# Optimization experiments

Hardware: AMD Instinct MI355X
Metric: run time of the kernel (lower is better)

The kernel has to match this reference:

```python
import math
import jax, jax.numpy as jnp
import numpy as np

H = 16  # head_count

def setup_inputs() -> dict:
    key = jax.random.key(0)
    ks = jax.random.split(key, 7)
    B, S, D = 2, 2048, 1024
    query = jax.random.normal(ks[0], (B, S, D), dtype=jnp.float32)
    # mask: True = masked position (matches masked_fill_ semantics)
    mask = jax.random.randint(ks[1], (B, S, S), 0, 2) > 0
    scale = 1.0 / math.sqrt(D)  # xavier-ish init scale
    Wq = jax.random.normal(ks[2], (D, D), dtype=jnp.float32) * scale
    Wk = jax.random.normal(ks[3], (D, D), dtype=jnp.float32) * scale
    Wv = jax.random.normal(ks[4], (D, D), dtype=jnp.float32) * scale
    Wo = jax.random.normal(ks[5], (D, D), dtype=jnp.float32) * scale
    bo = jnp.zeros((D,), dtype=jnp.float32)
    return {"query": query, "mask": mask, "Wq": Wq, "Wk": Wk, "Wv": Wv, "Wo": Wo, "bo": bo}


def reference(query, mask, Wq, Wk, Wv, Wo, bo):
    B, S, D = query.shape
    dh = D // H

    def split_heads(x):  # [B,S,D] -> [B,H,S,dh]
        return x.reshape(B, S, H, dh).transpose(0, 2, 1, 3)

    # torch nn.Linear computes x @ W.T (bias-free for q/k/v)
    q = split_heads(query @ Wq.T) * (1.0 / math.sqrt(dh))
    k = split_heads(query @ Wk.T)
    v = split_heads(query @ Wv.T)

    scores = jnp.einsum('bhqd,bhkd->bhqk', q, k)           # [B,H,S,S]
    scores = jnp.where(mask[:, None, :, :], jnp.float32(-1e18), scores)
    weights = jax.nn.softmax(scores, axis=-1)               # dropout=0 -> identity
    ctx = jnp.einsum('bhqk,bhkd->bhqd', weights, v)         # [B,H,S,dh]
    ctx = ctx.transpose(0, 2, 1, 3).reshape(B, S, D)        # combine heads
    return ctx @ Wo.T + bo
```

## Files before the change

### kernel.cpp

```cpp
#include <hip/hip_runtime.h>

#define S_LEN 2048
#define D_MODEL 1024
#define NH 16
#define DH 64

typedef __bf16 bf16x8 __attribute__((ext_vector_type(8)));
typedef __bf16 bf16x4 __attribute__((ext_vector_type(4)));
typedef float f32x4 __attribute__((ext_vector_type(4)));

__device__ __forceinline__ unsigned short f2bf(float f) {
  unsigned int x = __float_as_uint(f);
  x += 0x7fffu + ((x >> 16) & 1u);
  return (unsigned short)(x >> 16);
}

__device__ __forceinline__ bf16x4 cvt4(f32x4 v) {
  return __builtin_convertvector(v, bf16x4);
}

__device__ __forceinline__ float exp2raw(float x) {
#if __has_builtin(__builtin_amdgcn_exp2f)
  return __builtin_amdgcn_exp2f(x);
#else
  return exp2f(x);
#endif
}

__device__ __forceinline__ f32x4 mfma16(bf16x8 a, bf16x8 b, f32x4 c) {
  return __builtin_amdgcn_mfma_f32_16x16x32_bf16(a, b, c, 0, 0, 0);
}

__device__ __forceinline__ void gl2lds(const unsigned short* g, unsigned short* l) {
  __builtin_amdgcn_global_load_lds(
      (__attribute__((address_space(1))) void*)g,
      (__attribute__((address_space(3))) void*)l, 16, 0, 0);
}

__global__ __launch_bounds__(256) void prep_kernel(
    const float* __restrict__ q, const float* __restrict__ wq,
    const float* __restrict__ wk, const float* __restrict__ wv,
    const float* __restrict__ wo, const int* __restrict__ mask,
    unsigned short* __restrict__ qbf, unsigned short* __restrict__ wbf,
    unsigned long long* __restrict__ bits) {
  const int bx = blockIdx.x;
  if (bx < 32768) {
    int i = bx * 256 + threadIdx.x;
    unsigned long long bal = __ballot(mask[i] != 0);
    if ((threadIdx.x & 63) == 0) bits[i >> 6] = bal;
  } else {
    const long t = (long)(bx - 32768) * 256 + threadIdx.x;
    const float* src;
    unsigned short* dst;
    long e;
    if (t < 524288) { src = q; dst = qbf; e = t * 8; }
    else {
      long u = t - 524288;
      int wi = (int)(u >> 17);
      e = (u & 131071) * 8;
      src = wi == 0 ? wq : wi == 1 ? wk : wi == 2 ? wv : wo;
      dst = wbf + (long)wi * 1048576;
    }
    float4 a = *(const float4*)(src + e);
    float4 b = *(const float4*)(src + e + 4);
    ushort4 p0 = {f2bf(a.x), f2bf(a.y), f2bf(a.z), f2bf(a.w)};
    ushort4 p1 = {f2bf(b.x), f2bf(b.y), f2bf(b.z), f2bf(b.w)};
    *(ushort4*)(dst + e) = p0;
    *(ushort4*)(dst + e + 4) = p1;
  }
}

__global__ __launch_bounds__(256) void gemm_qkv(
    const unsigned short* __restrict__ A, const unsigned short* __restrict__ W3,
    unsigned short* __restrict__ qb, unsigned short* __restrict__ kb,
    unsigned short* __restrict__ vt, float qscale) {
  __shared__ unsigned short As[128 * 64];
  __shared__ unsigned short Bs[128 * 64];
  const int tid = threadIdx.x, lane = tid & 63, wid = tid >> 6;
  const int wm = wid >> 1, wn = wid & 1;
  const int quad = lane >> 4, c = lane & 15, cx = c & 7;
  const int nG = blockIdx.x * 128;
  const int wi = nG >> 10, nn0 = nG & 1023;
  const int m0 = blockIdx.y * 128;
  const unsigned short* Bsrc = W3 + (size_t)wi * 1048576;
  const int srow = lane >> 3;
  const int schk = ((lane & 7) ^ srow) * 8;
  const unsigned short* ag = A + (size_t)(m0 + wid * 32 + srow) * 1024 + schk;
  const unsigned short* bg = Bsrc + (size_t)(nn0 + wid * 32 + srow) * 1024 + schk;
  f32x4 acc[4][4] = {};
  for (int kk = 0; kk < 1024; kk += 64) {
#pragma unroll
    for (int i = 0; i < 4; ++i) {
      gl2lds(ag + (size_t)(i * 8) * 1024 + kk, &As[(wid * 32 + i * 8) * 64]);
      gl2lds(bg + (size_t)(i * 8) * 1024 + kk, &Bs[(wid * 32 + i * 8) * 64]);
    }
    __syncthreads();
#pragma unroll
    for (int kc = 0; kc < 2; ++kc) {
      bf16x8 a[4], b[4];
#pragma unroll
      for (int mt = 0; mt < 4; ++mt)
        a[mt] = *(const bf16x8*)(
            &As[(wm * 64 + mt * 16 + c) * 64 + ((kc * 4 + quad) ^ cx) * 8]);
#pragma unroll
      for (int nt = 0; nt < 4; ++nt)
        b[nt] = *(const bf16x8*)(
            &Bs[(wn * 64 + nt * 16 + c) * 64 + ((kc * 4 + quad) ^ cx) * 8]);
#pragma unroll
      for (int mt = 0; mt < 4; ++mt)
#pragma unroll
        for (int nt = 0; nt < 4; ++nt)
          acc[mt][nt] = mfma16(a[mt], b[nt], acc[mt][nt]);
    }
    __syncthreads();
  }
#pragma unroll
  for (int mt = 0; mt < 4; ++mt) {
#pragma unroll
    for (int nt = 0; nt < 4; ++nt) {
      const int mb = m0 + wm * 64 + mt * 16 + quad * 4;
      const int n = nn0 + wn * 64 + nt * 16 + c;
      const int hh = n >> 6, d = n & 63;
      const int bb = mb >> 11, ss = mb & 2047;
      if (wi == 0) {
#pragma unroll
        for (int r = 0; r < 4; ++r)
          qb[(size_t)((bb * NH + hh) * S_LEN + ss + r) * DH + d] =
              f2bf(acc[mt][nt][r] * qscale);
      } else if (wi == 1) {
#pragma unroll
        for (int r = 0; r < 4; ++r)
          kb[(size_t)((bb * NH + hh) * S_LEN + ss + r) * DH + d] =
              f2bf(acc[mt][nt][r]);
      } else {
        *(bf16x4*)(vt + (size_t)((bb * NH + hh) * DH + d) * S_LEN + ss) =
            cvt4(acc[mt][nt]);
      }
    }
  }
}

__global__ __launch_bounds__(256) void gemm_out(
    const unsigned short* __restrict__ A, const unsigned short* __restrict__ W,
    float* __restrict__ out, const float* __restrict__ bias) {
  __shared__ unsigned short As[128 * 64];
  __shared__ unsigned short Bs[64 * 64];
  const int tid = threadIdx.x, lane = tid & 63, wid = tid >> 6;
  const int wm = wid >> 1, wn = wid & 1;
  const int quad = lane >> 4, c = lane & 15, cx = c & 7;
  const int n0 = blockIdx.x * 64, m0 = blockIdx.y * 128;
  const int srow = lane >> 3;
  const int schk = ((lane & 7) ^ srow) * 8;
  const unsigned short* ag = A + (size_t)(m0 + wid * 32 + srow) * 1024 + schk;
  const unsigned short* bg = W + (size_t)(n0 + wid * 16 + srow) * 1024 + schk;
  f32x4 acc[4][2] = {};
  for (int kk = 0; kk < 1024; kk += 64) {
#pragma unroll
    for (int i = 0; i < 4; ++i)
      gl2lds(ag + (size_t)(i * 8) * 1024 + kk, &As[(wid * 32 + i * 8) * 64]);
#pragma unroll
    for (int i = 0; i < 2; ++i)
      gl2lds(bg + (size_t)(i * 8) * 1024 + kk, &Bs[(wid * 16 + i * 8) * 64]);
    __syncthreads();
#pragma unroll
    for (int kc = 0; kc < 2; ++kc) {
      bf16x8 a[4], b[2];
#pragma unroll
      for (int mt = 0; mt < 4; ++mt)
        a[mt] = *(const bf16x8*)(
            &As[(wm * 64 + mt * 16 + c) * 64 + ((kc * 4 + quad) ^ cx) * 8]);
#pragma unroll
      for (int nt = 0; nt < 2; ++nt)
        b[nt] = *(const bf16x8*)(
            &Bs[(wn * 32 + nt * 16 + c) * 64 + ((kc * 4 + quad) ^ cx) * 8]);
#pragma unroll
      for (int mt = 0; mt < 4; ++mt)
#pragma unroll
        for (int nt = 0; nt < 2; ++nt)
          acc[mt][nt] = mfma16(a[mt], b[nt], acc[mt][nt]);
    }
    __syncthreads();
  }
#pragma unroll
  for (int mt = 0; mt < 4; ++mt) {
#pragma unroll
    for (int nt = 0; nt < 2; ++nt) {
      const int mb = m0 + wm * 64 + mt * 16 + quad * 4;
      const int n = n0 + wn * 32 + nt * 16 + c;
      const float bv = bias[n];
#pragma unroll
      for (int r = 0; r < 4; ++r)
        out[(size_t)(mb + r) * D_MODEL + n] = acc[mt][nt][r] + bv;
    }
  }
}

__global__ __launch_bounds__(256, 2) void attn_kernel(
    const unsigned short* __restrict__ qb, const unsigned short* __restrict__ kb,
    const unsigned short* __restrict__ vt,
    const unsigned long long* __restrict__ mbits,
    unsigned short* __restrict__ ctx) {
  const int h = blockIdx.x, qt = blockIdx.y, b = blockIdx.z;
  const int bh = b * NH + h;
  const int tid = threadIdx.x, lane = tid & 63, wid = tid >> 6;
  const int quad = lane >> 4, c = lane & 15, cx = c & 7;
  const int qw = wid & 1, kh = wid >> 1;
  const int q0 = qt * 128;
  __shared__ __align__(16) unsigned short KV[4][4096];
  __shared__ __align__(16) unsigned short Pbuf[4][64 * 72];

  const int qbase = q0 + qw * 64;
  const unsigned short* qp = qb + (size_t)(bh * S_LEN + qbase + c) * DH;
  bf16x8 bq[4][2];
#pragma unroll
  for (int sub = 0; sub < 4; ++sub) {
    bq[sub][0] = *(const bf16x8*)(qp + sub * 16 * DH + quad * 8);
    bq[sub][1] = *(const bf16x8*)(qp + sub * 16 * DH + 32 + quad * 8);
  }

  f32x4 o[4][4] = {};
  float lacc[4] = {0.f, 0.f, 0.f, 0.f};
  const unsigned long long* mq0 =
      mbits + (size_t)(b * S_LEN + qbase + c) * 32 + kh * 16;

  const int srow = lane >> 3, schk = ((lane & 7) ^ srow) * 8;
  const unsigned short* Ksh = KV[kh];
  const unsigned short* Vsh = KV[2 + kh];
  unsigned short* Pw = Pbuf[wid];

  const unsigned short* gK =
      kb + (size_t)(bh * S_LEN + (wid & 1) * 1024 + srow) * DH + schk;
  const unsigned short* gV =
      vt + (size_t)(bh * DH + srow) * S_LEN + (wid - 2) * 1024 + schk;

  for (int kt = 0; kt < 1024; kt += 64) {
    if (wid < 2) {
#pragma unroll
      for (int i = 0; i < 8; ++i)
        gl2lds(gK + (size_t)(kt + i * 8) * DH, &KV[wid][i * 512]);
    } else {
#pragma unroll
      for (int i = 0; i < 8; ++i)
        gl2lds(gV + (size_t)(i * 8) * S_LEN + kt, &KV[wid][i * 512]);
    }
    __syncthreads();

    bf16x8 kf[8];
#pragma unroll
    for (int g = 0; g < 4; ++g) {
      const int rho = g * 16 + c;
      kf[2 * g] = *(const bf16x8*)(&Ksh[rho * 64 + (quad ^ cx) * 8]);
      kf[2 * g + 1] = *(const bf16x8*)(&Ksh[rho * 64 + ((4 + quad) ^ cx) * 8]);
    }

    const int mi = kt >> 6;
#pragma unroll
    for (int sub = 0; sub < 4; ++sub) {
      f32x4 s[4];
#pragma unroll
      for (int g = 0; g < 4; ++g) {
        f32x4 z = {};
        z = mfma16(kf[2 * g], bq[sub][0], z);
        z = mfma16(kf[2 * g + 1], bq[sub][1], z);
        s[g] = z;
      }
      const unsigned long long w64 = mq0[sub * 512 + mi];
      const unsigned int wlo = (unsigned int)w64;
      const unsigned int whi = (unsigned int)(w64 >> 32);
      float lp = 0.f;
#pragma unroll
      for (int g = 0; g < 4; ++g) {
        const unsigned int bits =
            ((g & 2) ? whi : wlo) >> ((g & 1) * 16 + quad * 4);
        f32x4 p;
#pragma unroll
        for (int r = 0; r < 4; ++r) {
          const float e = exp2raw(s[g][r]);
          p[r] = ((bits >> r) & 1u) ? 0.f : e;
          lp += p[r];
        }
        *(bf16x4*)(&Pw[(sub * 16 + c) * 72 + g * 16 + quad * 4]) = cvt4(p);
      }
      lacc[sub] += lp;
    }

#pragma unroll
    for (int ks = 0; ks < 2; ++ks) {
      bf16x8 bp[4];
#pragma unroll
      for (int sub = 0; sub < 4; ++sub)
        bp[sub] =
            *(const bf16x8*)(&Pw[(sub * 16 + c) * 72 + ks * 32 + quad * 8]);
#pragma unroll
      for (int nt = 0; nt < 4; ++nt) {
        bf16x8 av = *(const bf16x8*)(
            &Vsh[(nt * 16 + c) * 64 + ((ks * 4 + quad) ^ cx) * 8]);
#pragma unroll
        for (int sub = 0; sub < 4; ++sub)
          o[sub][nt] = mfma16(av, bp[sub], o[sub][nt]);
      }
    }
    __syncthreads();
  }

#pragma unroll
  for (int sub = 0; sub < 4; ++sub) {
    lacc[sub] += __shfl_xor(lacc[sub], 16, 64);
    lacc[sub] += __shfl_xor(lacc[sub], 32, 64);
  }

  float* mrg = (float*)&Pbuf[0][0];
  float* ml = mrg + 8 * 1088;
  if (kh == 1) {
#pragma unroll
    for (int sub = 0; sub < 4; ++sub) {
      float* mo = mrg + (qw * 4 + sub) * 1088;
#pragma unroll
      for (int nt = 0; nt < 4; ++nt)
        *(f32x4*)(mo + c * 68 + nt * 16 + quad * 4) = o[sub][nt];
      if (quad == 0) ml[(qw * 4 + sub) * 16 + c] = lacc[sub];
    }
  }
  __syncthreads();
  if (kh == 0) {
#pragma unroll
    for (int sub = 0; sub < 4; ++sub) {
      const int pp = qw * 4 + sub;
      const float inv = 1.0f / (lacc[sub] + ml[pp * 16 + c]);
      const int q = qbase + sub * 16 + c;
      const float* mo = mrg + pp * 1088;
#pragma unroll
      for (int nt = 0; nt < 4; ++nt) {
        f32x4 ob = *(const f32x4*)(mo + c * 68 + nt * 16 + quad * 4);
        f32x4 rr = (o[sub][nt] + ob) * inv;
        *(bf16x4*)(ctx + (size_t)(b * S_LEN + q) * D_MODEL + h * DH + nt * 16 +
                   quad * 4) = cvt4(rr);
      }
    }
  }
}

extern "C" void kernel_launch(void* const* d_in, const int* in_sizes, int n_in,
                              void* d_out, int out_size, void* d_ws, size_t ws_size,
                              hipStream_t stream) {
  const float* query = (const float*)d_in[0];
  const int* mask = (const int*)d_in[1];
  const float* Wq = (const float*)d_in[2];
  const float* Wk = (const float*)d_in[3];
  const float* Wv = (const float*)d_in[4];
  const float* Wo = (const float*)d_in[5];
  const float* bo = (const float*)d_in[6];
  float* out = (float*)d_out;

  char* ws = (char*)d_ws;
  const size_t MB = 1024 * 1024;
  unsigned short* qbf = (unsigned short*)(ws);
  unsigned short* wbf = (unsigned short*)(ws + 8 * MB);
  unsigned short* qb = (unsigned short*)(ws + 16 * MB);
  unsigned short* kb = (unsigned short*)(ws + 24 * MB);
  unsigned short* vt = (unsigned short*)(ws + 32 * MB);
  unsigned long long* mb = (unsigned long long*)(ws + 40 * MB);
  unsigned short* ctx = qbf;

  prep_kernel<<<32768 + 4096, 256, 0, stream>>>(query, Wq, Wk, Wv, Wo, mask,
                                                qbf, wbf, mb);

  gemm_qkv<<<dim3(3072 / 128, 4096 / 128), 256, 0, stream>>>(
      qbf, wbf, qb, kb, vt, 0.18033688f);

  attn_kernel<<<dim3(NH, S_LEN / 128, 2), 256, 0, stream>>>(qb, kb, vt, mb,
                                                            ctx);

  gemm_out<<<dim3(1024 / 64, 4096 / 128), 256, 0, stream>>>(
      ctx, wbf + 3 * 1048576, out, bo);
}
```

Baseline: 224.3 us.

## Double-buffer LDS tiles via register prefetch in GEMMs and attention

Replaces direct global-to-LDS loads with register-staged prefetch into double-buffered shared tiles in the QKV GEMM, the output GEMM and the attention kernel. This lets each iteration run on a single barrier and overlaps the next tile's global loads with MFMA work. The attention P scratch buffer shrinks to one 16-row slab per wave and is reused for each sub-tile. The merge area moves into the KV buffer, with an extra barrier before it. The cost is more VGPRs for the staging registers and twice the LDS for K/V and GEMM tiles, which may limit occupancy.

```diff
diff --git a/kernel.cpp b/kernel.cpp
--- a/kernel.cpp
+++ b/kernel.cpp
@@ -29,12 +29,6 @@
 
 __device__ __forceinline__ f32x4 mfma16(bf16x8 a, bf16x8 b, f32x4 c) {
   return __builtin_amdgcn_mfma_f32_16x16x32_bf16(a, b, c, 0, 0, 0);
-}
-
-__device__ __forceinline__ void gl2lds(const unsigned short* g, unsigned short* l) {
-  __builtin_amdgcn_global_load_lds(
-      (__attribute__((address_space(1))) void*)g,
-      (__attribute__((address_space(3))) void*)l, 16, 0, 0);
 }
 
 __global__ __launch_bounds__(256) void prep_kernel(
@@ -70,12 +64,12 @@
   }
 }
 
-__global__ __launch_bounds__(256) void gemm_qkv(
+__global__ __launch_bounds__(256, 2) void gemm_qkv(
     const unsigned short* __restrict__ A, const unsigned short* __restrict__ W3,
     unsigned short* __restrict__ qb, unsigned short* __restrict__ kb,
     unsigned short* __restrict__ vt, float qscale) {
-  __shared__ unsigned short As[128 * 64];
-  __shared__ unsigned short Bs[128 * 64];
+  __shared__ unsigned short As[2][128 * 64];
+  __shared__ unsigned short Bs[2][128 * 64];
   const int tid = threadIdx.x, lane = tid & 63, wid = tid >> 6;
   const int wm = wid >> 1, wn = wid & 1;
   const int quad = lane >> 4, c = lane & 15, cx = c & 7;
@@ -86,33 +80,49 @@
   const int srow = lane >> 3;
   const int schk = ((lane & 7) ^ srow) * 8;
   const unsigned short* ag = A + (size_t)(m0 + wid * 32 + srow) * 1024 + schk;
-  const unsigned short* bg = Bsrc + (size_t)(nn0 + wid * 32 + srow) * 1024 + schk;
+  const unsigned short* bg =
+      Bsrc + (size_t)(nn0 + wid * 32 + srow) * 1024 + schk;
   f32x4 acc[4][4] = {};
+  uint4 ra[4], rb[4];
+#pragma unroll
+  for (int i = 0; i < 4; ++i) {
+    ra[i] = *(const uint4*)(ag + (size_t)(i * 8) * 1024);
+    rb[i] = *(const uint4*)(bg + (size_t)(i * 8) * 1024);
+  }
   for (int kk = 0; kk < 1024; kk += 64) {
+    const int pb = (kk >> 6) & 1;
+    unsigned short* da = &As[pb][(wid * 32) * 64] + lane * 8;
+    unsigned short* db = &Bs[pb][(wid * 32) * 64] + lane * 8;
 #pragma unroll
     for (int i = 0; i < 4; ++i) {
-      gl2lds(ag + (size_t)(i * 8) * 1024 + kk, &As[(wid * 32 + i * 8) * 64]);
-      gl2lds(bg + (size_t)(i * 8) * 1024 + kk, &Bs[(wid * 32 + i * 8) * 64]);
+      *(uint4*)(da + i * 512) = ra[i];
+      *(uint4*)(db + i * 512) = rb[i];
     }
     __syncthreads();
+    if (kk + 64 < 1024) {
+#pragma unroll
+      for (int i = 0; i < 4; ++i) {
+        ra[i] = *(const uint4*)(ag + (size_t)(i * 8) * 1024 + kk + 64);
+        rb[i] = *(const uint4*)(bg + (size_t)(i * 8) * 1024 + kk + 64);
+      }
+    }
 #pragma unroll
     for (int kc = 0; kc < 2; ++kc) {
       bf16x8 a[4], b[4];
 #pragma unroll
       for (int mt = 0; mt < 4; ++mt)
         a[mt] = *(const bf16x8*)(
-            &As[(wm * 64 + mt * 16 + c) * 64 + ((kc * 4 + quad) ^ cx) * 8]);
+            &As[pb][(wm * 64 + mt * 16 + c) * 64 + ((kc * 4 + quad) ^ cx) * 8]);
 #pragma unroll
       for (int nt = 0; nt < 4; ++nt)
         b[nt] = *(const bf16x8*)(
-            &Bs[(wn * 64 + nt * 16 + c) * 64 + ((kc * 4 + quad) ^ cx) * 8]);
+            &Bs[pb][(wn * 64 + nt * 16 + c) * 64 + ((kc * 4 + quad) ^ cx) * 8]);
 #pragma unroll
       for (int mt = 0; mt < 4; ++mt)
 #pragma unroll
         for (int nt = 0; nt < 4; ++nt)
           acc[mt][nt] = mfma16(a[mt], b[nt], acc[mt][nt]);
     }
-    __syncthreads();
   }
 #pragma unroll
   for (int mt = 0; mt < 4; ++mt) {
@@ -140,11 +150,11 @@
   }
 }
 
-__global__ __launch_bounds__(256) void gemm_out(
+__global__ __launch_bounds__(256, 2) void gemm_out(
     const unsigned short* __restrict__ A, const unsigned short* __restrict__ W,
     float* __restrict__ out, const float* __restrict__ bias) {
-  __shared__ unsigned short As[128 * 64];
-  __shared__ unsigned short Bs[64 * 64];
+  __shared__ unsigned short As[2][128 * 64];
+  __shared__ unsigned short Bs[2][64 * 64];
   const int tid = threadIdx.x, lane = tid & 63, wid = tid >> 6;
   const int wm = wid >> 1, wn = wid & 1;
   const int quad = lane >> 4, c = lane & 15, cx = c & 7;
@@ -154,32 +164,47 @@
   const unsigned short* ag = A + (size_t)(m0 + wid * 32 + srow) * 1024 + schk;
   const unsigned short* bg = W + (size_t)(n0 + wid * 16 + srow) * 1024 + schk;
   f32x4 acc[4][2] = {};
+  uint4 ra[4], rb[2];
+#pragma unroll
+  for (int i = 0; i < 4; ++i)
+    ra[i] = *(const uint4*)(ag + (size_t)(i * 8) * 1024);
+#pragma unroll
+  for (int i = 0; i < 2; ++i)
+    rb[i] = *(const uint4*)(bg + (size_t)(i * 8) * 1024);
   for (int kk = 0; kk < 1024; kk += 64) {
-#pragma unroll
-    for (int i = 0; i < 4; ++i)
-      gl2lds(ag + (size_t)(i * 8) * 1024 + kk, &As[(wid * 32 + i * 8) * 64]);
-#pragma unroll
-    for (int i = 0; i < 2; ++i)
-      gl2lds(bg + (size_t)(i * 8) * 1024 + kk, &Bs[(wid * 16 + i * 8) * 64]);
+    const int pb = (kk >> 6) & 1;
+    unsigned short* da = &As[pb][(wid * 32) * 64] + lane * 8;
+    unsigned short* db = &Bs[pb][(wid * 16) * 64] + lane * 8;
+#pragma unroll
+    for (int i = 0; i < 4; ++i) *(uint4*)(da + i * 512) = ra[i];
+#pragma unroll
+    for (int i = 0; i < 2; ++i) *(uint4*)(db + i * 512) = rb[i];
     __syncthreads();
+    if (kk + 64 < 1024) {
+#pragma unroll
+      for (int i = 0; i < 4; ++i)
+        ra[i] = *(const uint4*)(ag + (size_t)(i * 8) * 1024 + kk + 64);
+#pragma unroll
+      for (int i = 0; i < 2; ++i)
+        rb[i] = *(const uint4*)(bg + (size_t)(i * 8) * 1024 + kk + 64);
+    }
 #pragma unroll
     for (int kc = 0; kc < 2; ++kc) {
       bf16x8 a[4], b[2];
 #pragma unroll
       for (int mt = 0; mt < 4; ++mt)
         a[mt] = *(const bf16x8*)(
-            &As[(wm * 64 + mt * 16 + c) * 64 + ((kc * 4 + quad) ^ cx) * 8]);
+            &As[pb][(wm * 64 + mt * 16 + c) * 64 + ((kc * 4 + quad) ^ cx) * 8]);
 #pragma unroll
       for (int nt = 0; nt < 2; ++nt)
         b[nt] = *(const bf16x8*)(
-            &Bs[(wn * 32 + nt * 16 + c) * 64 + ((kc * 4 + quad) ^ cx) * 8]);
+            &Bs[pb][(wn * 32 + nt * 16 + c) * 64 + ((kc * 4 + quad) ^ cx) * 8]);
 #pragma unroll
       for (int mt = 0; mt < 4; ++mt)
 #pragma unroll
         for (int nt = 0; nt < 2; ++nt)
           acc[mt][nt] = mfma16(a[mt], b[nt], acc[mt][nt]);
     }
-    __syncthreads();
   }
 #pragma unroll
   for (int mt = 0; mt < 4; ++mt) {
@@ -206,8 +231,8 @@
   const int quad = lane >> 4, c = lane & 15, cx = c & 7;
   const int qw = wid & 1, kh = wid >> 1;
   const int q0 = qt * 128;
-  __shared__ __align__(16) unsigned short KV[4][4096];
-  __shared__ __align__(16) unsigned short Pbuf[4][64 * 72];
+  __shared__ __align__(16) unsigned short KV[2][4][4096];
+  __shared__ __align__(16) unsigned short Pbuf[4][16 * 72];
 
   const int qbase = q0 + qw * 64;
   const unsigned short* qp = qb + (size_t)(bh * S_LEN + qbase + c) * DH;
@@ -223,27 +248,45 @@
   const unsigned long long* mq0 =
       mbits + (size_t)(b * S_LEN + qbase + c) * 32 + kh * 16;
 
-  const int srow = lane >> 3, schk = ((lane & 7) ^ srow) * 8;
-  const unsigned short* Ksh = KV[kh];
-  const unsigned short* Vsh = KV[2 + kh];
+  const int srow = lane >> 3;
+  const int schk = ((lane & 7) ^ srow) * 8;
   unsigned short* Pw = Pbuf[wid];
-
+  const bool isV = wid >= 2;
   const unsigned short* gK =
       kb + (size_t)(bh * S_LEN + (wid & 1) * 1024 + srow) * DH + schk;
   const unsigned short* gV =
       vt + (size_t)(bh * DH + srow) * S_LEN + (wid - 2) * 1024 + schk;
 
+  uint4 st[8];
+  if (!isV) {
+#pragma unroll
+    for (int i = 0; i < 8; ++i)
+      st[i] = *(const uint4*)(gK + (size_t)(i * 8) * DH);
+  } else {
+#pragma unroll
+    for (int i = 0; i < 8; ++i)
+      st[i] = *(const uint4*)(gV + (size_t)(i * 8) * S_LEN);
+  }
+
   for (int kt = 0; kt < 1024; kt += 64) {
-    if (wid < 2) {
-#pragma unroll
-      for (int i = 0; i < 8; ++i)
-        gl2lds(gK + (size_t)(kt + i * 8) * DH, &KV[wid][i * 512]);
-    } else {
-#pragma unroll
-      for (int i = 0; i < 8; ++i)
-        gl2lds(gV + (size_t)(i * 8) * S_LEN + kt, &KV[wid][i * 512]);
-    }
+    const int pb = (kt >> 6) & 1;
+    unsigned short* dstp = &KV[pb][wid][0] + lane * 8;
+#pragma unroll
+    for (int i = 0; i < 8; ++i) *(uint4*)(dstp + i * 512) = st[i];
     __syncthreads();
+    if (kt + 64 < 1024) {
+      if (!isV) {
+#pragma unroll
+        for (int i = 0; i < 8; ++i)
+          st[i] = *(const uint4*)(gK + (size_t)(kt + 64 + i * 8) * DH);
+      } else {
+#pragma unroll
+        for (int i = 0; i < 8; ++i)
+          st[i] = *(const uint4*)(gV + (size_t)(i * 8) * S_LEN + kt + 64);
+      }
+    }
+    const unsigned short* Ksh = &KV[pb][kh][0];
+    const unsigned short* Vsh = &KV[pb][2 + kh][0];
 
     bf16x8 kf[8];
 #pragma unroll
@@ -254,6 +297,7 @@
     }
 
     const int mi = kt >> 6;
+    bf16x8 bp[4][2];
 #pragma unroll
     for (int sub = 0; sub < 4; ++sub) {
       f32x4 s[4];
@@ -279,28 +323,24 @@
           p[r] = ((bits >> r) & 1u) ? 0.f : e;
           lp += p[r];
         }
-        *(bf16x4*)(&Pw[(sub * 16 + c) * 72 + g * 16 + quad * 4]) = cvt4(p);
+        *(bf16x4*)(&Pw[c * 72 + g * 16 + quad * 4]) = cvt4(p);
       }
       lacc[sub] += lp;
+      bp[sub][0] = *(const bf16x8*)(&Pw[c * 72 + quad * 8]);
+      bp[sub][1] = *(const bf16x8*)(&Pw[c * 72 + 32 + quad * 8]);
     }
 
 #pragma unroll
     for (int ks = 0; ks < 2; ++ks) {
-      bf16x8 bp[4];
-#pragma unroll
-      for (int sub = 0; sub < 4; ++sub)
-        bp[sub] =
-            *(const bf16x8*)(&Pw[(sub * 16 + c) * 72 + ks * 32 + quad * 8]);
 #pragma unroll
       for (int nt = 0; nt < 4; ++nt) {
         bf16x8 av = *(const bf16x8*)(
             &Vsh[(nt * 16 + c) * 64 + ((ks * 4 + quad) ^ cx) * 8]);
 #pragma unroll
         for (int sub = 0; sub < 4; ++sub)
-          o[sub][nt] = mfma16(av, bp[sub], o[sub][nt]);
-      }
-    }
-    __syncthreads();
+          o[sub][nt] = mfma16(av, bp[sub][ks], o[sub][nt]);
+      }
+    }
   }
 
 #pragma unroll
@@ -309,7 +349,8 @@
     lacc[sub] += __shfl_xor(lacc[sub], 32, 64);
   }
 
-  float* mrg = (float*)&Pbuf[0][0];
+  __syncthreads();
+  float* mrg = (float*)&KV[0][0][0];
   float* ml = mrg + 8 * 1088;
   if (kh == 1) {
 #pragma unroll
```

Measured after the change: 359.8 us. 60.4% more time.

## Give each wave private K/V LDS buffers and drop per-tile block barriers

Applied to the files above, without the earlier changes.

Each wave now loads its own K and V tiles into a private LDS region, replacing the shared loads split across waves, so the two __syncthreads per key tile become per-wave vmcnt/lgkmcnt waits. The next K tile is prefetched after QK^T and the next V tile after the PV MFMAs, which overlaps global-to-LDS traffic with compute. The P buffer shrinks to one 16-row slice per sub-tile. In exchange, global and LDS load traffic doubles because the pairs of waves sharing a key half each fetch it, and correctness now depends on the waitcnt ordering within a wave.

```diff
diff --git a/kernel.cpp b/kernel.cpp
--- a/kernel.cpp
+++ b/kernel.cpp
@@ -206,8 +206,8 @@
   const int quad = lane >> 4, c = lane & 15, cx = c & 7;
   const int qw = wid & 1, kh = wid >> 1;
   const int q0 = qt * 128;
-  __shared__ __align__(16) unsigned short KV[4][4096];
-  __shared__ __align__(16) unsigned short Pbuf[4][64 * 72];
+  __shared__ __align__(16) unsigned short KVw[4][8192];
+  __shared__ __align__(16) unsigned short Pbuf[4][16 * 72];
 
   const int qbase = q0 + qw * 64;
   const unsigned short* qp = qb + (size_t)(bh * S_LEN + qbase + c) * DH;
@@ -223,37 +223,36 @@
   const unsigned long long* mq0 =
       mbits + (size_t)(b * S_LEN + qbase + c) * 32 + kh * 16;
 
-  const int srow = lane >> 3, schk = ((lane & 7) ^ srow) * 8;
-  const unsigned short* Ksh = KV[kh];
-  const unsigned short* Vsh = KV[2 + kh];
+  const int srow = lane >> 3;
+  const int schk = ((lane & 7) ^ srow) * 8;
+  unsigned short* Kw = KVw[wid];
+  unsigned short* Vw = KVw[wid] + 4096;
   unsigned short* Pw = Pbuf[wid];
 
   const unsigned short* gK =
-      kb + (size_t)(bh * S_LEN + (wid & 1) * 1024 + srow) * DH + schk;
+      kb + (size_t)(bh * S_LEN + kh * 1024 + srow) * DH + schk;
   const unsigned short* gV =
-      vt + (size_t)(bh * DH + srow) * S_LEN + (wid - 2) * 1024 + schk;
+      vt + (size_t)(bh * DH + srow) * S_LEN + kh * 1024 + schk;
+
+#pragma unroll
+  for (int i = 0; i < 8; ++i) {
+    gl2lds(gK + (size_t)(i * 8) * DH, &Kw[i * 512]);
+    gl2lds(gV + (size_t)(i * 8) * S_LEN, &Vw[i * 512]);
+  }
 
   for (int kt = 0; kt < 1024; kt += 64) {
-    if (wid < 2) {
-#pragma unroll
-      for (int i = 0; i < 8; ++i)
-        gl2lds(gK + (size_t)(kt + i * 8) * DH, &KV[wid][i * 512]);
-    } else {
-#pragma unroll
-      for (int i = 0; i < 8; ++i)
-        gl2lds(gV + (size_t)(i * 8) * S_LEN + kt, &KV[wid][i * 512]);
-    }
-    __syncthreads();
+    asm volatile("s_waitcnt vmcnt(0)" ::: "memory");
 
     bf16x8 kf[8];
 #pragma unroll
     for (int g = 0; g < 4; ++g) {
       const int rho = g * 16 + c;
-      kf[2 * g] = *(const bf16x8*)(&Ksh[rho * 64 + (quad ^ cx) * 8]);
-      kf[2 * g + 1] = *(const bf16x8*)(&Ksh[rho * 64 + ((4 + quad) ^ cx) * 8]);
+      kf[2 * g] = *(const bf16x8*)(&Kw[rho * 64 + (quad ^ cx) * 8]);
+      kf[2 * g + 1] = *(const bf16x8*)(&Kw[rho * 64 + ((4 + quad) ^ cx) * 8]);
     }
 
     const int mi = kt >> 6;
+    bf16x8 bp[4][2];
 #pragma unroll
     for (int sub = 0; sub < 4; ++sub) {
       f32x4 s[4];
@@ -279,28 +278,36 @@
           p[r] = ((bits >> r) & 1u) ? 0.f : e;
           lp += p[r];
         }
-        *(bf16x4*)(&Pw[(sub * 16 + c) * 72 + g * 16 + quad * 4]) = cvt4(p);
+        *(bf16x4*)(&Pw[c * 72 + g * 16 + quad * 4]) = cvt4(p);
       }
       lacc[sub] += lp;
+      bp[sub][0] = *(const bf16x8*)(&Pw[c * 72 + quad * 8]);
+      bp[sub][1] = *(const bf16x8*)(&Pw[c * 72 + 32 + quad * 8]);
+    }
+
+    if (kt + 64 < 1024) {
+#pragma unroll
+      for (int i = 0; i < 8; ++i)
+        gl2lds(gK + (size_t)(kt + 64 + i * 8) * DH, &Kw[i * 512]);
     }
 
 #pragma unroll
     for (int ks = 0; ks < 2; ++ks) {
-      bf16x8 bp[4];
-#pragma unroll
-      for (int sub = 0; sub < 4; ++sub)
-        bp[sub] =
-            *(const bf16x8*)(&Pw[(sub * 16 + c) * 72 + ks * 32 + quad * 8]);
 #pragma unroll
       for (int nt = 0; nt < 4; ++nt) {
         bf16x8 av = *(const bf16x8*)(
-            &Vsh[(nt * 16 + c) * 64 + ((ks * 4 + quad) ^ cx) * 8]);
+            &Vw[(nt * 16 + c) * 64 + ((ks * 4 + quad) ^ cx) * 8]);
 #pragma unroll
         for (int sub = 0; sub < 4; ++sub)
-          o[sub][nt] = mfma16(av, bp[sub], o[sub][nt]);
-      }
-    }
-    __syncthreads();
+          o[sub][nt] = mfma16(av, bp[sub][ks], o[sub][nt]);
+      }
+    }
+    asm volatile("s_waitcnt lgkmcnt(0)" ::: "memory");
+    if (kt + 64 < 1024) {
+#pragma unroll
+      for (int i = 0; i < 8; ++i)
+        gl2lds(gV + (size_t)(i * 8) * S_LEN + kt + 64, &Vw[i * 512]);
+    }
   }
 
 #pragma unroll
@@ -309,7 +316,8 @@
     lacc[sub] += __shfl_xor(lacc[sub], 32, 64);
   }
 
-  float* mrg = (float*)&Pbuf[0][0];
+  __syncthreads();
+  float* mrg = (float*)&KVw[0][0];
   float* ml = mrg + 8 * 1088;
   if (kh == 1) {
 #pragma unroll
```

After: 226.4 us. No clear change (+0.9%).
